# Kernel tuning notes

Measured on AMD Instinct MI355X. Metric: run time of the kernel, lower is better.

## Reference

```python
import jax, jax.numpy as jnp
import numpy as np


def setup_inputs() -> dict:
    key = jax.random.key(0)
    k0, k1, k2, k3 = jax.random.split(key, 4)
    B, C, E, K = 2, 16, 400000, 10
    x = jax.random.normal(k0, (B, C, E, 1), dtype=jnp.float32)
    Gi = jax.random.randint(k1, (B, E, K), 0, E)  # 1-ring neighbor edge ids
    # Conv2d(32 -> 1, kernel 1x1) == a length-32 weight vector + scalar bias.
    conv_w = jax.random.normal(k2, (2 * C,), dtype=jnp.float32) * 0.1
    conv_b = jnp.zeros((), dtype=jnp.float32)
    rconv_w = jax.random.normal(k3, (2 * C,), dtype=jnp.float32) * 0.1
    rconv_b = jnp.zeros((), dtype=jnp.float32)
    return {"x": x, "Gi": Gi, "conv_w": conv_w, "conv_b": conv_b,
            "rconv_w": rconv_w, "rconv_b": rconv_b}


def reference(x, Gi, conv_w, conv_b, rconv_w, rconv_b):
    TOPK = 4
    x = x[..., 0]                      # (B, C, E)
    B, C, E = x.shape
    # create_GeMM: prepend a zero "padding edge" at index 0, shift indices by 1.
    x_pad = jnp.concatenate([jnp.zeros((B, C, 1), x.dtype), x], axis=2)  # (B,C,E+1)
    idx = Gi + 1                       # (B, E, K)
    # Gather neighbor features: G[b,c,e,k] = x_pad[b,c,idx[b,e,k]]
    G = jax.vmap(lambda xp, i: xp[:, i])(x_pad, idx)   # (B, C, E, K)
    K = G.shape[-1]
    # conv over cat([repeated original, sampled], dim=channel): split the 1x1
    # conv weight into the half acting on x and the half acting on G (no concat
    # materialization needed).
    sim = jax.nn.sigmoid(
        jnp.einsum('bcek,c->bek', G, conv_w[C:])
        + jnp.einsum('bce,c->be', x, conv_w[:C])[..., None]
        + conv_b)                       # (B, E, K)
    _, inds = jax.lax.top_k(sim, TOPK)  # (B, E, 4), largest first (as torch.topk)
    inds_exp = jnp.broadcast_to(inds[:, None], (B, C, E, TOPK))
    topk_feat = jnp.take_along_axis(G, inds_exp, axis=-1)  # (B, C, E, 4)
    rw = jax.nn.sigmoid(
        jnp.einsum('bcek,c->bek', topk_feat, rconv_w[C:])
        + jnp.einsum('bce,c->be', x, rconv_w[:C])[..., None]
        + rconv_b)                      # (B, E, 4)
    summed = jnp.sum(topk_feat * rw[:, None], axis=-1)     # (B, C, E)
    return x + summed
```

## Files before the change

### kernel.cpp

```cpp
#include <hip/hip_runtime.h>
#include <math.h>

#define NCH 16
#define KNB 10
#define NTOP 4

__global__ __launch_bounds__(256) void prep_kernel(
    const float* __restrict__ x, const float* __restrict__ conv_w,
    float* __restrict__ xT, float* __restrict__ d, int E)
{
    const int b = blockIdx.y;
    const int q = blockIdx.x * blockDim.x + threadIdx.x;
    const int e0 = q * 4;
    if (e0 >= E) return;

    float wcg[NCH];
#pragma unroll
    for (int c = 0; c < NCH; ++c) wcg[c] = conv_w[NCH + c];

    const float* xb = x + (size_t)b * NCH * E;
    float4 v[NCH];
#pragma unroll
    for (int c = 0; c < NCH; ++c)
        v[c] = *(const float4*)(xb + (size_t)c * E + e0);

    float* rowb = xT + ((size_t)b * E + e0) * NCH;
#pragma unroll
    for (int i = 0; i < 4; ++i) {
        float4* dst = (float4*)(rowb + (size_t)i * NCH);
        dst[0] = make_float4(i==0?v[0].x:i==1?v[0].y:i==2?v[0].z:v[0].w,
                             i==0?v[1].x:i==1?v[1].y:i==2?v[1].z:v[1].w,
                             i==0?v[2].x:i==1?v[2].y:i==2?v[2].z:v[2].w,
                             i==0?v[3].x:i==1?v[3].y:i==2?v[3].z:v[3].w);
        dst[1] = make_float4(i==0?v[4].x:i==1?v[4].y:i==2?v[4].z:v[4].w,
                             i==0?v[5].x:i==1?v[5].y:i==2?v[5].z:v[5].w,
                             i==0?v[6].x:i==1?v[6].y:i==2?v[6].z:v[6].w,
                             i==0?v[7].x:i==1?v[7].y:i==2?v[7].z:v[7].w);
        dst[2] = make_float4(i==0?v[8].x:i==1?v[8].y:i==2?v[8].z:v[8].w,
                             i==0?v[9].x:i==1?v[9].y:i==2?v[9].z:v[9].w,
                             i==0?v[10].x:i==1?v[10].y:i==2?v[10].z:v[10].w,
                             i==0?v[11].x:i==1?v[11].y:i==2?v[11].z:v[11].w);
        dst[3] = make_float4(i==0?v[12].x:i==1?v[12].y:i==2?v[12].z:v[12].w,
                             i==0?v[13].x:i==1?v[13].y:i==2?v[13].z:v[13].w,
                             i==0?v[14].x:i==1?v[14].y:i==2?v[14].z:v[14].w,
                             i==0?v[15].x:i==1?v[15].y:i==2?v[15].z:v[15].w);
    }

    float d0, d1, d2, d3;
    {
#pragma clang fp contract(off)
        float s0 = 0.0f, s1 = 0.0f, s2 = 0.0f, s3 = 0.0f;
#pragma unroll
        for (int c = 0; c < NCH; ++c) {
            s0 = s0 + v[c].x * wcg[c];
            s1 = s1 + v[c].y * wcg[c];
            s2 = s2 + v[c].z * wcg[c];
            s3 = s3 + v[c].w * wcg[c];
        }
        d0 = s0; d1 = s1; d2 = s2; d3 = s3;
    }
    *(float4*)(d + (size_t)b * E + e0) = make_float4(d0, d1, d2, d3);
}

__global__ __launch_bounds__(256) void atten_kernel(
    const float* __restrict__ xT,
    const float* __restrict__ d,
    const int*   __restrict__ Gi,
    const float* __restrict__ conv_w,
    const float* __restrict__ conv_b,
    const float* __restrict__ rconv_w,
    const float* __restrict__ rconv_b,
    float*       __restrict__ out,
    int E)
{
    const int b = blockIdx.y;
    const int e = blockIdx.x * blockDim.x + threadIdx.x;
    if (e >= E) return;

    float wcx[NCH], wrx[NCH], wrg[NCH];
#pragma unroll
    for (int c = 0; c < NCH; ++c) {
        wcx[c] = conv_w[c];
        wrx[c] = rconv_w[c];
        wrg[c] = rconv_w[NCH + c];
    }
    const float  cb32 = conv_b[0];
    const double rb   = (double)rconv_b[0];

    const float4* xrow = (const float4*)(xT + ((size_t)b * E + e) * NCH);
    float xe[NCH];
#pragma unroll
    for (int i = 0; i < 4; ++i) {
        float4 t = xrow[i];
        xe[4*i+0] = t.x; xe[4*i+1] = t.y; xe[4*i+2] = t.z; xe[4*i+3] = t.w;
    }

    float sX_c;
    {
#pragma clang fp contract(off)
        float s = 0.0f;
#pragma unroll
        for (int c = 0; c < NCH; ++c) s = s + xe[c] * wcx[c];
        sX_c = s;
    }
    double xs_r = rb;
#pragma unroll
    for (int c = 0; c < NCH; ++c) xs_r += (double)xe[c] * (double)wrx[c];

    const int2* gi2 = (const int2*)(Gi + ((size_t)b * E + e) * KNB);
    int j[KNB];
#pragma unroll
    for (int k = 0; k < 5; ++k) {
        int2 t = gi2[k];
        j[2*k+0] = t.x; j[2*k+1] = t.y;
    }

    const float* db = d + (size_t)b * E;
    float dk[KNB];
#pragma unroll
    for (int k = 0; k < KNB; ++k) dk[k] = db[j[k]];

    float sim[KNB];
#pragma unroll
    for (int k = 0; k < KNB; ++k) {
        float l = (dk[k] + sX_c) + cb32;
        float t = (float)exp(-(double)l);
        sim[k] = 1.0f / (1.0f + t);
    }

    float acc[NCH];
#pragma unroll
    for (int c = 0; c < NCH; ++c) acc[c] = 0.f;

    unsigned used = 0;
#pragma unroll
    for (int t = 0; t < NTOP; ++t) {
        float best = -INFINITY; int bi = 0; int bj = 0;
#pragma unroll
        for (int k = 0; k < KNB; ++k) {
            const bool ok = !(used & (1u << k)) && (sim[k] > best);
            best = ok ? sim[k] : best;
            bi   = ok ? k      : bi;
            bj   = ok ? j[k]   : bj;
        }
        used |= 1u << bi;

        const float4* grow = (const float4*)(xT + ((size_t)b * E + bj) * NCH);
        float g[NCH];
#pragma unroll
        for (int i = 0; i < 4; ++i) {
            float4 gv = grow[i];
            g[4*i+0] = gv.x; g[4*i+1] = gv.y; g[4*i+2] = gv.z; g[4*i+3] = gv.w;
        }
        double r = xs_r;
#pragma unroll
        for (int c = 0; c < NCH; ++c) r += (double)g[c] * (double)wrg[c];
        const float rw = (float)(1.0 / (1.0 + exp(-r)));
#pragma unroll
        for (int c = 0; c < NCH; ++c) acc[c] += g[c] * rw;
    }

    float* ob = out + (size_t)b * NCH * E;
#pragma unroll
    for (int c = 0; c < NCH; ++c) ob[(size_t)c * E + e] = xe[c] + acc[c];
}

extern "C" void kernel_launch(void* const* d_in, const int* in_sizes, int n_in,
                              void* d_out, int out_size, void* d_ws, size_t ws_size,
                              hipStream_t stream) {
    const float* x       = (const float*)d_in[0];
    const int*   Gi      = (const int*)  d_in[1];
    const float* conv_w  = (const float*)d_in[2];
    const float* conv_b  = (const float*)d_in[3];
    const float* rconv_w = (const float*)d_in[4];
    const float* rconv_b = (const float*)d_in[5];
    float*       out     = (float*)d_out;

    const int B = 2;
    const int E = in_sizes[1] / (B * KNB);

    float* xT = (float*)d_ws;
    float* dt = (float*)d_ws + (size_t)B * E * NCH;

    dim3 blk(256, 1, 1);
    dim3 grd_p(((E / 4) + 255) / 256, B, 1);
    prep_kernel<<<grd_p, blk, 0, stream>>>(x, conv_w, xT, dt, E);

    dim3 grd_a((E + 255) / 256, B, 1);
    atten_kernel<<<grd_a, blk, 0, stream>>>(xT, dt, Gi, conv_w, conv_b,
                                            rconv_w, rconv_b, out, E);
}
```

Measured before the change: 254.6 us.

## Store gathered neighbor features as bf16 and batch top-k row loads

The transposed per-edge feature table is now stored in bf16 instead of fp32, which halves the bytes moved by the random neighbor gathers. The prep kernel transposes through shared memory. The attention kernel reads the edge's own features directly from the original channel-major input, issues all four top-k row loads together, and swaps the double-precision reweighting sigmoid for fp32 with fast exp. The trade-off is lower precision in the gathered features and in the reweighting sum, which could push outputs past tolerance.

```diff
diff --git a/kernel.cpp b/kernel.cpp
--- a/kernel.cpp
+++ b/kernel.cpp
@@ -1,77 +1,85 @@
 #include <hip/hip_runtime.h>
 #include <math.h>
 
-#define NCH 16
-#define KNB 10
+#define NCH  16
+#define KNB  10
 #define NTOP 4
+#define TILE 512
+#define PADE 514
+
+__device__ __forceinline__ unsigned short f32_to_bf16_rne(float f) {
+    unsigned u = __float_as_uint(f);
+    u += 0x7FFFu + ((u >> 16) & 1u);
+    return (unsigned short)(u >> 16);
+}
+__device__ __forceinline__ float bf16_to_f32(unsigned us) {
+    return __uint_as_float(us << 16);
+}
 
 __global__ __launch_bounds__(256) void prep_kernel(
     const float* __restrict__ x, const float* __restrict__ conv_w,
-    float* __restrict__ xT, float* __restrict__ d, int E)
+    unsigned short* __restrict__ xTb, float* __restrict__ d, int E)
 {
-    const int b = blockIdx.y;
-    const int q = blockIdx.x * blockDim.x + threadIdx.x;
-    const int e0 = q * 4;
-    if (e0 >= E) return;
+    __shared__ float lds[NCH * PADE];
+    const int b  = blockIdx.y;
+    const int e0 = blockIdx.x * TILE;
+    const int t  = threadIdx.x;
+    const int rem = min(TILE, E - e0);
 
     float wcg[NCH];
 #pragma unroll
     for (int c = 0; c < NCH; ++c) wcg[c] = conv_w[NCH + c];
 
-    const float* xb = x + (size_t)b * NCH * E;
-    float4 v[NCH];
-#pragma unroll
-    for (int c = 0; c < NCH; ++c)
-        v[c] = *(const float4*)(xb + (size_t)c * E + e0);
-
-    float* rowb = xT + ((size_t)b * E + e0) * NCH;
-#pragma unroll
-    for (int i = 0; i < 4; ++i) {
-        float4* dst = (float4*)(rowb + (size_t)i * NCH);
-        dst[0] = make_float4(i==0?v[0].x:i==1?v[0].y:i==2?v[0].z:v[0].w,
-                             i==0?v[1].x:i==1?v[1].y:i==2?v[1].z:v[1].w,
-                             i==0?v[2].x:i==1?v[2].y:i==2?v[2].z:v[2].w,
-                             i==0?v[3].x:i==1?v[3].y:i==2?v[3].z:v[3].w);
-        dst[1] = make_float4(i==0?v[4].x:i==1?v[4].y:i==2?v[4].z:v[4].w,
-                             i==0?v[5].x:i==1?v[5].y:i==2?v[5].z:v[5].w,
-                             i==0?v[6].x:i==1?v[6].y:i==2?v[6].z:v[6].w,
-                             i==0?v[7].x:i==1?v[7].y:i==2?v[7].z:v[7].w);
-        dst[2] = make_float4(i==0?v[8].x:i==1?v[8].y:i==2?v[8].z:v[8].w,
-                             i==0?v[9].x:i==1?v[9].y:i==2?v[9].z:v[9].w,
-                             i==0?v[10].x:i==1?v[10].y:i==2?v[10].z:v[10].w,
-                             i==0?v[11].x:i==1?v[11].y:i==2?v[11].z:v[11].w);
-        dst[3] = make_float4(i==0?v[12].x:i==1?v[12].y:i==2?v[12].z:v[12].w,
-                             i==0?v[13].x:i==1?v[13].y:i==2?v[13].z:v[13].w,
-                             i==0?v[14].x:i==1?v[14].y:i==2?v[14].z:v[14].w,
-                             i==0?v[15].x:i==1?v[15].y:i==2?v[15].z:v[15].w);
-    }
-
-    float d0, d1, d2, d3;
-    {
+    const float* xb = x + (size_t)b * NCH * E + e0;
+    if (2 * t + 1 < rem) {
+#pragma unroll
+        for (int c = 0; c < NCH; ++c) {
+            float2 v = *(const float2*)(xb + (size_t)c * E + 2 * t);
+            lds[c * PADE + 2 * t]     = v.x;
+            lds[c * PADE + 2 * t + 1] = v.y;
+        }
+    }
+    __syncthreads();
+
+#pragma unroll
+    for (int rr = 0; rr < 2; ++rr) {
+        const int row = t + rr * 256;
+        if (row < rem) {
 #pragma clang fp contract(off)
-        float s0 = 0.0f, s1 = 0.0f, s2 = 0.0f, s3 = 0.0f;
-#pragma unroll
-        for (int c = 0; c < NCH; ++c) {
-            s0 = s0 + v[c].x * wcg[c];
-            s1 = s1 + v[c].y * wcg[c];
-            s2 = s2 + v[c].z * wcg[c];
-            s3 = s3 + v[c].w * wcg[c];
-        }
-        d0 = s0; d1 = s1; d2 = s2; d3 = s3;
-    }
-    *(float4*)(d + (size_t)b * E + e0) = make_float4(d0, d1, d2, d3);
+            float s = 0.0f;
+#pragma unroll
+            for (int c = 0; c < NCH; ++c) s = s + lds[c * PADE + row] * wcg[c];
+            d[(size_t)b * E + e0 + row] = s;
+        }
+    }
+
+    unsigned short* outb = xTb + ((size_t)b * E + e0) * NCH;
+#pragma unroll
+    for (int r = 0; r < 4; ++r) {
+        const int f = t + r * 256;
+        const int row = f >> 1, h = f & 1;
+        if (row < rem) {
+            float v[8];
+#pragma unroll
+            for (int k = 0; k < 8; ++k) v[k] = lds[(h * 8 + k) * PADE + row];
+            uint4 pk;
+            pk.x = (unsigned)f32_to_bf16_rne(v[0]) | ((unsigned)f32_to_bf16_rne(v[1]) << 16);
+            pk.y = (unsigned)f32_to_bf16_rne(v[2]) | ((unsigned)f32_to_bf16_rne(v[3]) << 16);
+            pk.z = (unsigned)f32_to_bf16_rne(v[4]) | ((unsigned)f32_to_bf16_rne(v[5]) << 16);
+            pk.w = (unsigned)f32_to_bf16_rne(v[6]) | ((unsigned)f32_to_bf16_rne(v[7]) << 16);
+            *(uint4*)(outb + (size_t)f * 8) = pk;
+        }
+    }
 }
 
 __global__ __launch_bounds__(256) void atten_kernel(
-    const float* __restrict__ xT,
-    const float* __restrict__ d,
-    const int*   __restrict__ Gi,
-    const float* __restrict__ conv_w,
-    const float* __restrict__ conv_b,
-    const float* __restrict__ rconv_w,
-    const float* __restrict__ rconv_b,
-    float*       __restrict__ out,
-    int E)
+    const float*          __restrict__ x,
+    const unsigned short* __restrict__ xTb,
+    const float*          __restrict__ d,
+    const int*            __restrict__ Gi,
+    const float* __restrict__ conv_w,  const float* __restrict__ conv_b,
+    const float* __restrict__ rconv_w, const float* __restrict__ rconv_b,
+    float* __restrict__ out, int E)
 {
     const int b = blockIdx.y;
     const int e = blockIdx.x * blockDim.x + threadIdx.x;
@@ -84,16 +92,13 @@
         wrx[c] = rconv_w[c];
         wrg[c] = rconv_w[NCH + c];
     }
-    const float  cb32 = conv_b[0];
-    const double rb   = (double)rconv_b[0];
-
-    const float4* xrow = (const float4*)(xT + ((size_t)b * E + e) * NCH);
+    const float cb32 = conv_b[0];
+    const float rb32 = rconv_b[0];
+
+    const float* xb = x + (size_t)b * NCH * E;
     float xe[NCH];
 #pragma unroll
-    for (int i = 0; i < 4; ++i) {
-        float4 t = xrow[i];
-        xe[4*i+0] = t.x; xe[4*i+1] = t.y; xe[4*i+2] = t.z; xe[4*i+3] = t.w;
-    }
+    for (int c = 0; c < NCH; ++c) xe[c] = xb[(size_t)c * E + e];
 
     float sX_c;
     {
@@ -103,16 +108,16 @@
         for (int c = 0; c < NCH; ++c) s = s + xe[c] * wcx[c];
         sX_c = s;
     }
-    double xs_r = rb;
-#pragma unroll
-    for (int c = 0; c < NCH; ++c) xs_r += (double)xe[c] * (double)wrx[c];
+    float xs_r = rb32;
+#pragma unroll
+    for (int c = 0; c < NCH; ++c) xs_r = fmaf(xe[c], wrx[c], xs_r);
 
     const int2* gi2 = (const int2*)(Gi + ((size_t)b * E + e) * KNB);
     int j[KNB];
 #pragma unroll
     for (int k = 0; k < 5; ++k) {
-        int2 t = gi2[k];
-        j[2*k+0] = t.x; j[2*k+1] = t.y;
+        int2 t2 = gi2[k];
+        j[2 * k + 0] = t2.x; j[2 * k + 1] = t2.y;
     }
 
     const float* db = d + (size_t)b * E;
@@ -128,10 +133,7 @@
         sim[k] = 1.0f / (1.0f + t);
     }
 
-    float acc[NCH];
-#pragma unroll
-    for (int c = 0; c < NCH; ++c) acc[c] = 0.f;
-
+    int bjv[NTOP];
     unsigned used = 0;
 #pragma unroll
     for (int t = 0; t < NTOP; ++t) {
@@ -144,20 +146,37 @@
             bj   = ok ? j[k]   : bj;
         }
         used |= 1u << bi;
-
-        const float4* grow = (const float4*)(xT + ((size_t)b * E + bj) * NCH);
+        bjv[t] = bj;
+    }
+
+    uint4 ga[NTOP], gb[NTOP];
+#pragma unroll
+    for (int t = 0; t < NTOP; ++t) {
+        const uint4* p = (const uint4*)(xTb + ((size_t)b * E + bjv[t]) * NCH);
+        ga[t] = p[0]; gb[t] = p[1];
+    }
+
+    float acc[NCH];
+#pragma unroll
+    for (int c = 0; c < NCH; ++c) acc[c] = 0.f;
+
+#pragma unroll
+    for (int t = 0; t < NTOP; ++t) {
         float g[NCH];
-#pragma unroll
-        for (int i = 0; i < 4; ++i) {
-            float4 gv = grow[i];
-            g[4*i+0] = gv.x; g[4*i+1] = gv.y; g[4*i+2] = gv.z; g[4*i+3] = gv.w;
-        }
-        double r = xs_r;
-#pragma unroll
-        for (int c = 0; c < NCH; ++c) r += (double)g[c] * (double)wrg[c];
-        const float rw = (float)(1.0 / (1.0 + exp(-r)));
-#pragma unroll
-        for (int c = 0; c < NCH; ++c) acc[c] += g[c] * rw;
+        g[0]  = bf16_to_f32(ga[t].x & 0xFFFFu); g[1]  = bf16_to_f32(ga[t].x >> 16);
+        g[2]  = bf16_to_f32(ga[t].y & 0xFFFFu); g[3]  = bf16_to_f32(ga[t].y >> 16);
+        g[4]  = bf16_to_f32(ga[t].z & 0xFFFFu); g[5]  = bf16_to_f32(ga[t].z >> 16);
+        g[6]  = bf16_to_f32(ga[t].w & 0xFFFFu); g[7]  = bf16_to_f32(ga[t].w >> 16);
+        g[8]  = bf16_to_f32(gb[t].x & 0xFFFFu); g[9]  = bf16_to_f32(gb[t].x >> 16);
+        g[10] = bf16_to_f32(gb[t].y & 0xFFFFu); g[11] = bf16_to_f32(gb[t].y >> 16);
+        g[12] = bf16_to_f32(gb[t].z & 0xFFFFu); g[13] = bf16_to_f32(gb[t].z >> 16);
+        g[14] = bf16_to_f32(gb[t].w & 0xFFFFu); g[15] = bf16_to_f32(gb[t].w >> 16);
+        float r = xs_r;
+#pragma unroll
+        for (int c = 0; c < NCH; ++c) r = fmaf(g[c], wrg[c], r);
+        const float rw = 1.0f / (1.0f + __expf(-r));
+#pragma unroll
+        for (int c = 0; c < NCH; ++c) acc[c] = fmaf(g[c], rw, acc[c]);
     }
 
     float* ob = out + (size_t)b * NCH * E;
@@ -179,14 +198,14 @@
     const int B = 2;
     const int E = in_sizes[1] / (B * KNB);
 
-    float* xT = (float*)d_ws;
-    float* dt = (float*)d_ws + (size_t)B * E * NCH;
+    unsigned short* xTb = (unsigned short*)d_ws;
+    float* dt = (float*)((char*)d_ws + (size_t)B * E * NCH * 2);
 
     dim3 blk(256, 1, 1);
-    dim3 grd_p(((E / 4) + 255) / 256, B, 1);
-    prep_kernel<<<grd_p, blk, 0, stream>>>(x, conv_w, xT, dt, E);
+    dim3 grd_p((E + TILE - 1) / TILE, B, 1);
+    prep_kernel<<<grd_p, blk, 0, stream>>>(x, conv_w, xTb, dt, E);
 
     dim3 grd_a((E + 255) / 256, B, 1);
-    atten_kernel<<<grd_a, blk, 0, stream>>>(xT, dt, Gi, conv_w, conv_b,
+    atten_kernel<<<grd_a, blk, 0, stream>>>(x, xTb, dt, Gi, conv_w, conv_b,
                                             rconv_w, rconv_b, out, E);
 }
```

After: 215.2 us. -15.5%, faster.
